# Performance work log

Measured on AMD Instinct MI355X. Metric: run time of the kernel, lower is better.

The kernel has to match this reference:

```python
import jax, jax.numpy as jnp
import numpy as np

NDIGIT = 10
DIM_IN = 256
DIM_OUT = 784
BATCH = 16384


def setup_inputs() -> dict:
    key = jax.random.key(0)
    k_theta, k_label, k_W = jax.random.split(key, 3)
    theta = jax.random.normal(k_theta, (BATCH, DIM_IN), dtype=jnp.float32)
    label = jax.random.randint(k_label, (BATCH,), 0, NDIGIT, dtype=jnp.int32)
    # xavier_uniform for each (dim_out, dim_in) matrix
    limit = float(np.sqrt(6.0 / (DIM_IN + DIM_OUT)))
    megaW = jax.random.uniform(k_W, (NDIGIT, DIM_OUT, DIM_IN), dtype=jnp.float32,
                               minval=-limit, maxval=limit)
    megab = jnp.zeros((NDIGIT, DIM_OUT), dtype=jnp.float32)
    return {"theta": theta, "label": label, "megaW": megaW, "megab": megab}


def reference(theta, label, megaW, megab):
    # Dense compute across all 10 digit experts (matches torch.bmm over repeated theta)
    # added: [b, ndigit, dim_out]
    added = jnp.einsum('ndi,bi->bnd', megaW, theta) + megab[None, :, :]
    # Select the expert output per example by label (vector_gather)
    selected = jnp.take_along_axis(added, label[:, None, None].astype(jnp.int32), axis=1)[:, 0, :]
    probs = jax.nn.sigmoid(selected)
    return probs
```

## Files before the change

kernel.cpp:

```cpp
#include <hip/hip_runtime.h>
#include <hip/hip_bf16.h>

#define NDIGIT 10
#define DIM_IN 256
#define DIM_OUT 784
#define BATCH 16384
#define BM 64
#define BN 112
#define NCB 7
#define MAX_MT (BATCH / BM + NDIGIT)
#define G_BLOCKS (MAX_MT * NCB)
#define QB 14336
#define RBSTRIDE 116
#define LDS_BYTES 29696

#define WS_IDX 1024
#define WS_DESC 600
#define WS_WBF_BYTES 69632
#define WS_TH_BYTES (WS_WBF_BYTES + 2007040 * 2)
#define WS_NEED (WS_TH_BYTES + BATCH * DIM_IN * 2)

typedef __attribute__((ext_vector_type(4))) float f32x4;
typedef __attribute__((ext_vector_type(8))) short bf16x8;

__device__ __forceinline__ short f2bf(float f) {
    union { float f; unsigned u; } c; c.f = f;
    unsigned u = c.u;
    u += 0x7fffu + ((u >> 16) & 1u);
    return (short)(u >> 16);
}

__device__ __forceinline__ void gload16(const void* gp, void* lp) {
    __builtin_amdgcn_global_load_lds(
        (const __attribute__((address_space(1))) void*)gp,
        (__attribute__((address_space(3))) void*)lp, 16, 0, 0);
}

__global__ void prep_k(const float* __restrict__ megaW,
                       const int* __restrict__ label,
                       int* __restrict__ wsi,
                       short* __restrict__ wbf) {
    int b = blockIdx.x, t = threadIdx.x;
    if (b < 980) {
        int base = b * 2048 + t * 8;
        f32x4 v0 = *(const f32x4*)(megaW + base);
        f32x4 v1 = *(const f32x4*)(megaW + base + 4);
        bf16x8 o;
        o[0] = f2bf(v0[0]); o[1] = f2bf(v0[1]); o[2] = f2bf(v0[2]); o[3] = f2bf(v0[3]);
        o[4] = f2bf(v1[0]); o[5] = f2bf(v1[1]); o[6] = f2bf(v1[2]); o[7] = f2bf(v1[3]);
        *(bf16x8*)(wbf + base) = o;
    } else {
        __shared__ int h[NDIGIT];
        int j = b - 980;
        if (t < NDIGIT) h[t] = 0;
        __syncthreads();
        int i0 = j * 512;
        atomicAdd(&h[label[i0 + t]], 1);
        atomicAdd(&h[label[i0 + 256 + t]], 1);
        __syncthreads();
        if (t < NDIGIT) wsi[64 + j * 16 + t] = h[t];
    }
}

__global__ void scatter2_k(const int* __restrict__ label, int* __restrict__ wsi) {
    __shared__ int tot[NDIGIT], bef[NDIGIT], base[NDIGIT + 1], cur[NDIGIT], toff[NDIGIT + 1];
    int j = blockIdx.x, t = threadIdx.x;
    if (t < NDIGIT) {
        int s = 0, sb = 0;
        for (int jj = 0; jj < 32; ++jj) {
            int v = wsi[64 + jj * 16 + t];
            s += v;
            if (jj < j) sb += v;
        }
        tot[t] = s; bef[t] = sb;
    }
    __syncthreads();
    if (t == 0) {
        int off = 0, tf = 0;
        for (int g = 0; g < NDIGIT; ++g) {
            base[g] = off; toff[g] = tf;
            off += tot[g]; tf += (tot[g] + BM - 1) / BM;
        }
        base[NDIGIT] = off; toff[NDIGIT] = tf;
    }
    __syncthreads();
    if (t < NDIGIT) cur[t] = base[t] + bef[t];
    if (j == 0) {
        int ptotal = toff[NDIGIT];
        for (int p = t; p < ptotal; p += 512) {
            int g2 = 0;
            while (p >= toff[g2 + 1]) ++g2;
            int row0 = (p - toff[g2]) * BM;
            int rcv = tot[g2] - row0; if (rcv > BM) rcv = BM;
            wsi[WS_DESC + p] = (base[g2] + row0) | (rcv << 14) | (g2 << 21);
        }
        if (t < NDIGIT) { wsi[t] = base[t]; wsi[12 + t] = toff[t]; }
        if (t == 0) {
            wsi[10] = base[NDIGIT]; wsi[22] = toff[NDIGIT]; wsi[24] = toff[NDIGIT];
        }
    }
    __syncthreads();
    int i = j * 512 + t;
    int g = label[i];
    int r = atomicAdd(&cur[g], 1);
    wsi[WS_IDX + r] = i;
}

__global__ void gth_k(const float* __restrict__ theta,
                      const int* __restrict__ wsi,
                      short* __restrict__ thsort) {
    int gid = blockIdx.x * 256 + threadIdx.x;
    int r = gid >> 5;
    int c8 = (gid & 31) << 3;
    int src = wsi[WS_IDX + r];
    const float* p = theta + (size_t)src * DIM_IN + c8;
    f32x4 v0 = *(const f32x4*)p;
    f32x4 v1 = *(const f32x4*)(p + 4);
    bf16x8 o;
    o[0] = f2bf(v0[0]); o[1] = f2bf(v0[1]); o[2] = f2bf(v0[2]); o[3] = f2bf(v0[3]);
    o[4] = f2bf(v1[0]); o[5] = f2bf(v1[1]); o[6] = f2bf(v1[2]); o[7] = f2bf(v1[3]);
    *(bf16x8*)(thsort + (size_t)r * DIM_IN + c8) = o;
}

__device__ __forceinline__ void stage_q(const char* Wcb, int q, char* Bq, int tid) {
#pragma unroll
    for (int it = 0; it < 4; ++it) {
        int chunk = it * 256 + tid;
        if (chunk >= 896) chunk -= 128;
        int lbyte = chunk << 4;
        int L = lbyte ^ ((((lbyte >> 7) & 7)) << 4);
        int row = L >> 7, koff = L & 127;
        gload16(Wcb + row * 512 + q * 128 + koff, Bq + lbyte);
    }
}

#define COMPUTE_Q(Q, BUF) do {                                                 \
    _Pragma("unroll")                                                          \
    for (int ksl = 0; ksl < 2; ++ksl) {                                        \
        _Pragma("unroll")                                                      \
        for (int ns = 0; ns < NCB; ++ns) {                                     \
            int n_ = ns * 16 + r16;                                            \
            int byte_ = (n_ << 7) + (ksl << 6) + (kg << 4);                    \
            byte_ ^= (n_ & 7) << 4;                                            \
            bf16x8 bfr_ = *(const bf16x8*)((const char*)(BUF) + byte_);        \
            acc[ns] = __builtin_amdgcn_mfma_f32_16x16x32_bf16(                 \
                a[(Q) * 2 + ksl], bfr_, acc[ns], 0, 0, 0);                     \
        }                                                                      \
    }                                                                          \
} while (0)

__launch_bounds__(256, 4)
__global__ void moe_gemm11_k(const short* __restrict__ thsort,
                             const float* __restrict__ megab,
                             const int* __restrict__ wsi,
                             const short* __restrict__ wbf,
                             float* __restrict__ out) {
    __shared__ char Bs[LDS_BYTES];

    int Bid = blockIdx.x;
    const int q8 = G_BLOCKS / 8, r8 = G_BLOCKS % 8;
    int xcd = Bid & 7, slot = Bid >> 3;
    int w = (xcd < r8 ? xcd * (q8 + 1) : r8 * (q8 + 1) + (xcd - r8) * q8) + slot;
    int mt = w / NCB, cb = w % NCB;

    int total = wsi[24];
    if (mt >= total) return;

    int d = wsi[WS_DESC + mt];
    int startRow = d & 0x3FFF;
    int rc = (d >> 14) & 0x7F;
    int g  = d >> 21;

    int tid = threadIdx.x;
    int wv = tid >> 6, l = tid & 63, r16 = l & 15, kg = l >> 4;

    const char* Wcb = (const char*)(wbf + ((size_t)g * DIM_OUT + (size_t)cb * BN) * DIM_IN);

    stage_q(Wcb, 0, Bs, tid);
    stage_q(Wcb, 1, Bs + QB, tid);

    int mloc = wv * 16 + r16; if (mloc >= rc) mloc = rc - 1;
    const short* Ar = thsort + (size_t)(startRow + mloc) * DIM_IN + kg * 8;
    bf16x8 a[8];
#pragma unroll
    for (int ks = 0; ks < 8; ++ks)
        a[ks] = *(const bf16x8*)(Ar + ks * 32);

    f32x4 acc[NCB];
#pragma unroll
    for (int ns = 0; ns < NCB; ++ns) acc[ns] = (f32x4){0.f, 0.f, 0.f, 0.f};

    __syncthreads();
    COMPUTE_Q(0, Bs);
    COMPUTE_Q(1, Bs + QB);
    __syncthreads();

    stage_q(Wcb, 2, Bs, tid);
    stage_q(Wcb, 3, Bs + QB, tid);
    __syncthreads();
    COMPUTE_Q(2, Bs);
    COMPUTE_Q(3, Bs + QB);

    const float* bg = megab + (size_t)g * DIM_OUT + (size_t)cb * BN;

    __syncthreads();

    float* rowbuf = (float*)Bs + wv * (16 * RBSTRIDE);
#pragma unroll
    for (int ns = 0; ns < NCB; ++ns) {
        int nloc = ns * 16 + r16;
        float bias = bg[nloc];
#pragma unroll
        for (int j = 0; j < 4; ++j) {
            float x = acc[ns][j] + bias;
            rowbuf[(kg * 4 + j) * RBSTRIDE + nloc] = 1.0f / (1.0f + __expf(-x));
        }
    }

    __syncthreads();

    const int* idxw = wsi + WS_IDX + startRow + wv * 16;
#pragma unroll
    for (int t = 0; t < 7; ++t) {
        int c = t * 64 + l;
        int row = c / 28;
        int cir = c - row * 28;
        if (wv * 16 + row < rc) {
            f32x4 v = *(const f32x4*)(rowbuf + row * RBSTRIDE + cir * 4);
            int orow = idxw[row];
            *(f32x4*)(out + (size_t)orow * DIM_OUT + cb * BN + cir * 4) = v;
        }
    }
}

__launch_bounds__(256, 4)
__global__ void moe_gemm4_k(const float* __restrict__ theta,
                            const float* __restrict__ megab,
                            const int* __restrict__ wsi,
                            const short* __restrict__ wbf,
                            float* __restrict__ out) {
    __shared__ short Bsf[BN * 128];
    int Bid = blockIdx.x;
    const int q8 = G_BLOCKS / 8, r8 = G_BLOCKS % 8;
    int xcd = Bid & 7, slot = Bid >> 3;
    int w = (xcd < r8 ? xcd * (q8 + 1) : r8 * (q8 + 1) + (xcd - r8) * q8) + slot;
    int mt = w / NCB, cb = w % NCB;
    int total = wsi[24];
    if (mt >= total) return;
    int g = 0;
    while (mt >= wsi[12 + g + 1]) ++g;
    int lt    = mt - wsi[12 + g];
    int start = wsi[g];
    int cnt   = wsi[g + 1] - start;
    int row0  = lt * BM;
    int rc    = min(BM, cnt - row0);
    int tid = threadIdx.x;
    int wv = tid >> 6, l = tid & 63, r16 = l & 15, kg = l >> 4;
    const char* Wcb = (const char*)(wbf + ((size_t)g * DIM_OUT + (size_t)cb * BN) * DIM_IN);
#pragma unroll
    for (int it = 0; it < 7; ++it) {
        int lbyte = (it * 256 + tid) << 4;
        int L = lbyte ^ (((lbyte >> 8) & 7) << 4);
        int srcoff = ((L >> 8) << 9) + (L & 255);
        gload16(Wcb + srcoff, (char*)Bsf + lbyte);
    }
    const int* idxlist = wsi + WS_IDX + start + row0;
    int mloc = wv * 16 + r16;
    int asrc = (mloc < rc) ? idxlist[mloc] : idxlist[0];
    const float* Arow = theta + (size_t)asrc * DIM_IN;
    bf16x8 a[8];
#pragma unroll
    for (int ks = 0; ks < 8; ++ks) {
        int k0 = ks * 32 + kg * 8;
        f32x4 v0 = *(const f32x4*)(Arow + k0);
        f32x4 v1 = *(const f32x4*)(Arow + k0 + 4);
        bf16x8 af;
        af[0] = f2bf(v0[0]); af[1] = f2bf(v0[1]);
        af[2] = f2bf(v0[2]); af[3] = f2bf(v0[3]);
        af[4] = f2bf(v1[0]); af[5] = f2bf(v1[1]);
        af[6] = f2bf(v1[2]); af[7] = f2bf(v1[3]);
        a[ks] = af;
    }
    f32x4 acc[NCB];
#pragma unroll
    for (int ns = 0; ns < NCB; ++ns) acc[ns] = (f32x4){0.f, 0.f, 0.f, 0.f};
    __syncthreads();
#pragma unroll
    for (int ks = 0; ks < 4; ++ks)
#pragma unroll
        for (int ns = 0; ns < NCB; ++ns) {
            int n = ns * 16 + r16;
            int byte = (n << 8) + (ks << 6) + (kg << 4);
            byte ^= (n & 7) << 4;
            bf16x8 b = *(const bf16x8*)((const char*)Bsf + byte);
            acc[ns] = __builtin_amdgcn_mfma_f32_16x16x32_bf16(a[ks], b, acc[ns], 0, 0, 0);
        }
    __syncthreads();
#pragma unroll
    for (int it = 0; it < 7; ++it) {
        int lbyte = (it * 256 + tid) << 4;
        int L = lbyte ^ (((lbyte >> 8) & 7) << 4);
        int srcoff = ((L >> 8) << 9) + (L & 255) + 256;
        gload16(Wcb + srcoff, (char*)Bsf + lbyte);
    }
    __syncthreads();
#pragma unroll
    for (int ks = 0; ks < 4; ++ks)
#pragma unroll
        for (int ns = 0; ns < NCB; ++ns) {
            int n = ns * 16 + r16;
            int byte = (n << 8) + (ks << 6) + (kg << 4);
            byte ^= (n & 7) << 4;
            bf16x8 b = *(const bf16x8*)((const char*)Bsf + byte);
            acc[ns] = __builtin_amdgcn_mfma_f32_16x16x32_bf16(a[4 + ks], b, acc[ns], 0, 0, 0);
        }
    const float* bg = megab + (size_t)g * DIM_OUT + (size_t)cb * BN;
    int rbase = wv * 16 + kg * 4;
    int orow[4];
#pragma unroll
    for (int j = 0; j < 4; ++j)
        orow[j] = (rbase + j < rc) ? idxlist[rbase + j] : -1;
#pragma unroll
    for (int ns = 0; ns < NCB; ++ns) {
        int nloc = ns * 16 + r16;
        float bias = bg[nloc];
#pragma unroll
        for (int j = 0; j < 4; ++j) {
            if (orow[j] >= 0) {
                float x = acc[ns][j] + bias;
                out[(size_t)orow[j] * DIM_OUT + cb * BN + nloc] = 1.0f / (1.0f + __expf(-x));
            }
        }
    }
}

extern "C" void kernel_launch(void* const* d_in, const int* in_sizes, int n_in,
                              void* d_out, int out_size, void* d_ws, size_t ws_size,
                              hipStream_t stream) {
    const float* theta = (const float*)d_in[0];
    const int*   label = (const int*)d_in[1];
    const float* megaW = (const float*)d_in[2];
    const float* megab = (const float*)d_in[3];
    float* out = (float*)d_out;
    int* wsi = (int*)d_ws;
    short* wbf = (short*)((char*)d_ws + WS_WBF_BYTES);

    prep_k    <<<1012, 256, 0, stream>>>(megaW, label, wsi, wbf);
    scatter2_k<<<32, 512, 0, stream>>>(label, wsi);

    if (ws_size >= (size_t)WS_NEED) {
        short* thsort = (short*)((char*)d_ws + WS_TH_BYTES);
        gth_k      <<<2048, 256, 0, stream>>>(theta, wsi, thsort);
        moe_gemm11_k<<<G_BLOCKS, 256, 0, stream>>>(thsort, megab, wsi, wbf, out);
    } else {
        moe_gemm4_k<<<G_BLOCKS, 256, 0, stream>>>(theta, megab, wsi, wbf, out);
    }
}
```

Measured before the change: 43.31 us.

## Halve GEMM LDS footprint with single-buffer staging and two-pass epilogue

The GEMM kernel now uses one 14 KB LDS buffer instead of two, staging and computing each K quarter in turn, with barriers between quarters. The sigmoid epilogue writes eight rows per wave per pass over two passes, so it fits in the smaller buffer. Launch bounds rise from 4 to 8 blocks per CU. The aim is more resident blocks to hide latency, at the cost of losing the double-staged overlap and adding more synchronisation.

```diff
diff --git a/kernel.cpp b/kernel.cpp
--- a/kernel.cpp
+++ b/kernel.cpp
@@ -12,7 +12,8 @@
 #define G_BLOCKS (MAX_MT * NCB)
 #define QB 14336
 #define RBSTRIDE 116
-#define LDS_BYTES 29696
+#define RBWAVE (8 * RBSTRIDE * 4)
+#define LDS_BYTES 14848
 
 #define WS_IDX 1024
 #define WS_DESC 600
@@ -134,7 +135,7 @@
     }
 }
 
-#define COMPUTE_Q(Q, BUF) do {                                                 \
+#define COMPUTE_Q(Q) do {                                                      \
     _Pragma("unroll")                                                          \
     for (int ksl = 0; ksl < 2; ++ksl) {                                        \
         _Pragma("unroll")                                                      \
@@ -142,15 +143,15 @@
             int n_ = ns * 16 + r16;                                            \
             int byte_ = (n_ << 7) + (ksl << 6) + (kg << 4);                    \
             byte_ ^= (n_ & 7) << 4;                                            \
-            bf16x8 bfr_ = *(const bf16x8*)((const char*)(BUF) + byte_);        \
+            bf16x8 bfr_ = *(const bf16x8*)(Bs + byte_);                        \
             acc[ns] = __builtin_amdgcn_mfma_f32_16x16x32_bf16(                 \
                 a[(Q) * 2 + ksl], bfr_, acc[ns], 0, 0, 0);                     \
         }                                                                      \
     }                                                                          \
 } while (0)
 
-__launch_bounds__(256, 4)
-__global__ void moe_gemm11_k(const short* __restrict__ thsort,
+__launch_bounds__(256, 8)
+__global__ void moe_gemm12_k(const short* __restrict__ thsort,
                              const float* __restrict__ megab,
                              const int* __restrict__ wsi,
                              const short* __restrict__ wbf,
@@ -176,9 +177,6 @@
 
     const char* Wcb = (const char*)(wbf + ((size_t)g * DIM_OUT + (size_t)cb * BN) * DIM_IN);
 
-    stage_q(Wcb, 0, Bs, tid);
-    stage_q(Wcb, 1, Bs + QB, tid);
-
     int mloc = wv * 16 + r16; if (mloc >= rc) mloc = rc - 1;
     const short* Ar = thsort + (size_t)(startRow + mloc) * DIM_IN + kg * 8;
     bf16x8 a[8];
@@ -190,45 +188,52 @@
 #pragma unroll
     for (int ns = 0; ns < NCB; ++ns) acc[ns] = (f32x4){0.f, 0.f, 0.f, 0.f};
 
-    __syncthreads();
-    COMPUTE_Q(0, Bs);
-    COMPUTE_Q(1, Bs + QB);
-    __syncthreads();
-
-    stage_q(Wcb, 2, Bs, tid);
-    stage_q(Wcb, 3, Bs + QB, tid);
-    __syncthreads();
-    COMPUTE_Q(2, Bs);
-    COMPUTE_Q(3, Bs + QB);
+#pragma unroll
+    for (int q = 0; q < 4; ++q) {
+        stage_q(Wcb, q, Bs, tid);
+        __syncthreads();
+        COMPUTE_Q(q);
+        __syncthreads();
+    }
 
     const float* bg = megab + (size_t)g * DIM_OUT + (size_t)cb * BN;
-
-    __syncthreads();
-
-    float* rowbuf = (float*)Bs + wv * (16 * RBSTRIDE);
-#pragma unroll
-    for (int ns = 0; ns < NCB; ++ns) {
-        int nloc = ns * 16 + r16;
-        float bias = bg[nloc];
-#pragma unroll
-        for (int j = 0; j < 4; ++j) {
-            float x = acc[ns][j] + bias;
-            rowbuf[(kg * 4 + j) * RBSTRIDE + nloc] = 1.0f / (1.0f + __expf(-x));
-        }
-    }
-
-    __syncthreads();
-
+    float* rowbuf = (float*)(Bs + wv * RBWAVE);
     const int* idxw = wsi + WS_IDX + startRow + wv * 16;
-#pragma unroll
-    for (int t = 0; t < 7; ++t) {
-        int c = t * 64 + l;
-        int row = c / 28;
-        int cir = c - row * 28;
-        if (wv * 16 + row < rc) {
-            f32x4 v = *(const f32x4*)(rowbuf + row * RBSTRIDE + cir * 4);
-            int orow = idxw[row];
-            *(f32x4*)(out + (size_t)orow * DIM_OUT + cb * BN + cir * 4) = v;
+    int kgp = kg >> 1;
+
+#pragma unroll
+    for (int p = 0; p < 2; ++p) {
+        if (p == 1) {
+            asm volatile("s_waitcnt lgkmcnt(0)" ::: "memory");
+            __builtin_amdgcn_sched_barrier(0);
+        }
+        if (kgp == p) {
+            int rb8 = (kg & 1) * 4;
+#pragma unroll
+            for (int ns = 0; ns < NCB; ++ns) {
+                int nloc = ns * 16 + r16;
+                float bias = bg[nloc];
+#pragma unroll
+                for (int j = 0; j < 4; ++j) {
+                    float x = acc[ns][j] + bias;
+                    rowbuf[(rb8 + j) * RBSTRIDE + nloc] = 1.0f / (1.0f + __expf(-x));
+                }
+            }
+        }
+        asm volatile("s_waitcnt lgkmcnt(0)" ::: "memory");
+        __builtin_amdgcn_sched_barrier(0);
+#pragma unroll
+        for (int t = 0; t < 4; ++t) {
+            int c = t * 64 + l;
+            if (c < 224) {
+                int row = c / 28;
+                int cir = c - row * 28;
+                int rl = p * 8 + row;
+                if (wv * 16 + rl < rc) {
+                    f32x4 v = *(const f32x4*)(rowbuf + row * RBSTRIDE + cir * 4);
+                    *(f32x4*)(out + (size_t)idxw[rl] * DIM_OUT + cb * BN + cir * 4) = v;
+                }
+            }
         }
     }
 }
@@ -350,8 +355,8 @@
 
     if (ws_size >= (size_t)WS_NEED) {
         short* thsort = (short*)((char*)d_ws + WS_TH_BYTES);
-        gth_k      <<<2048, 256, 0, stream>>>(theta, wsi, thsort);
-        moe_gemm11_k<<<G_BLOCKS, 256, 0, stream>>>(thsort, megab, wsi, wbf, out);
+        gth_k       <<<2048, 256, 0, stream>>>(theta, wsi, thsort);
+        moe_gemm12_k<<<G_BLOCKS, 256, 0, stream>>>(thsort, megab, wsi, wbf, out);
     } else {
         moe_gemm4_k<<<G_BLOCKS, 256, 0, stream>>>(theta, megab, wsi, wbf, out);
     }
```

Result: slower. 64.26 us (+48.4%).
